# Optimization experiments

Hardware: AMD Instinct MI355X
Metric: run time of the kernel (lower is better)

## Reference

```python
import jax, jax.numpy as jnp
import numpy as np

PATCH_SIZE = 14.0
PIXEL_THRESHOLD = 5.0


def setup_inputs() -> dict:
    key = jax.random.key(0)
    k1, k2, k3, k4, k5 = jax.random.split(key, 5)
    B, N = 32, 1024
    src_pts = jax.random.uniform(k1, (B, N, 2), dtype=jnp.float32) * 32.0  # patch coords
    tar_pts = jax.random.uniform(k2, (B, N, 2), dtype=jnp.float32) * 32.0
    scores = jax.random.uniform(k3, (B, N), dtype=jnp.float32)
    relScale = 0.5 + jax.random.uniform(k4, (B, N), dtype=jnp.float32)  # positive scales
    theta = jax.random.uniform(k5, (B, N), dtype=jnp.float32) * 2.0 * np.pi
    relInplane = jnp.stack([jnp.cos(theta), jnp.sin(theta)], axis=-1)  # (B,N,2) cos,sin
    return {"src_pts": src_pts, "tar_pts": tar_pts, "scores": scores,
            "relScale": relScale, "relInplane": relInplane}


def _ransac_single(src, tar, score, scale, inplane):
    # src, tar: (N,2); score, scale: (N,); inplane: (N,2) = (cos, sin)
    N = src.shape[0]
    valid = src[:, 0] != -1.0  # (N,) sentinel mask from original forward
    s = src * PATCH_SIZE
    t = tar * PATCH_SIZE
    c, si = inplane[:, 0], inplane[:, 1]
    # R = [[c, -s], [s, c]] per candidate -> (N,2,2)
    R = jnp.stack([jnp.stack([c, -si], -1), jnp.stack([si, c], -1)], -2)
    A = scale[:, None, None] * R                          # (N,2,2) linear part
    trans = t - jnp.einsum('nij,nj->ni', A, s)            # (N,2) translation so A@s_n + t_n == t_n
    # candidate n applied to every point m (leave-one-out handled by masking diag)
    pred = jnp.einsum('nij,mj->nmi', A, s) + trans[:, None, :]   # (N,N,2)
    err = jnp.linalg.norm(pred - t[None, :, :], axis=-1)          # (N,N)
    not_self = ~jnp.eye(N, dtype=bool)
    inlier = (err <= PIXEL_THRESHOLD) & valid[None, :] & not_self  # (N,N)
    score_inl = jnp.sum(inlier * score[None, :], axis=1)           # (N,)
    score_inl = jnp.where(valid, score_inl, -1.0)
    best = jnp.argmax(score_inl)
    failed = score_inl[best] == 0.0
    M = (jnp.eye(3, dtype=src.dtype)
         .at[:2, :2].set(A[best])
         .at[:2, 2].set(trans[best]))
    # pack inliers of best candidate to the front (original index order preserved)
    inl = inlier[best]                                   # (N,) bool
    order = jnp.argsort(jnp.where(inl, 0, 1), stable=True)
    cnt = jnp.sum(inl)
    keep = jnp.arange(N) < cnt
    out_src = jnp.where(keep[:, None], src[order], -1.0)
    out_tar = jnp.where(keep[:, None], tar[order], -1.0)
    out_sc = jnp.where(keep, score[order], 0.0)
    return M, failed, out_src, out_tar, out_sc


def reference(src_pts, tar_pts, scores, relScale, relInplane):
    Ms, failed, inl_src, inl_tar, inl_sc = jax.vmap(_ransac_single)(
        src_pts, tar_pts, scores, relScale, relInplane)
    return Ms, failed, inl_src, inl_tar, inl_sc
```

## Files before the change

### kernel.cpp

```cpp
#include <hip/hip_runtime.h>

constexpr int BB = 32;
constexpr int NN = 1024;
constexpr int SPLIT = 16;
constexpr int HYP = 128;
#define PATCH 14.0f
#define THRSQ 25.0f

__global__ __launch_bounds__(1024) void ransac_score_kernel(
    const float* __restrict__ src, const float* __restrict__ tar,
    const float* __restrict__ scores, const float* __restrict__ relScale,
    const float* __restrict__ relInplane, float* __restrict__ score_inl)
{
#pragma clang fp contract(off)
    const int blocksPerBatch = NN / HYP;
    const int b   = blockIdx.x / blocksPerBatch;
    const int g   = blockIdx.x % blocksPerBatch;
    const int tid = threadIdx.x;
    const int wave = tid >> 6;
    const int lane = tid & 63;

    __shared__ float4 pts[NN];
    __shared__ float  sc[NN];
    __shared__ float  partial[SPLIT][HYP];

    const float* srcb = src + (size_t)b * NN * 2;
    const float* tarb = tar + (size_t)b * NN * 2;
    const float* scb  = scores + (size_t)b * NN;

    for (int i = tid; i < NN; i += 1024) {
        float2 s = ((const float2*)srcb)[i];
        float2 t = ((const float2*)tarb)[i];
        pts[i] = make_float4(s.x * PATCH, s.y * PATCH, t.x * PATCH, t.y * PATCH);
        sc[i]  = (s.x != -1.0f) ? scb[i] : 0.0f;
    }
    __syncthreads();

    const int n0l = lane, n1l = lane + 64;
    const size_t base = (size_t)b * NN + (size_t)g * HYP;

    const float sc0v = relScale[base + n0l];
    const float sc1v = relScale[base + n1l];
    const float2 ip0 = ((const float2*)relInplane)[base + n0l];
    const float2 ip1 = ((const float2*)relInplane)[base + n1l];

    const float a00_0 = sc0v * ip0.x, a01_0 = sc0v * (-ip0.y);
    const float a10_0 = sc0v * ip0.y, a11_0 = sc0v * ip0.x;
    const float a00_1 = sc1v * ip1.x, a01_1 = sc1v * (-ip1.y);
    const float a10_1 = sc1v * ip1.y, a11_1 = sc1v * ip1.x;

    const float4 P0 = pts[g * HYP + n0l];
    const float4 P1 = pts[g * HYP + n1l];
    const float trx0 = P0.z - (a00_0 * P0.x + a01_0 * P0.y);
    const float try0 = P0.w - (a10_0 * P0.x + a11_0 * P0.y);
    const float trx1 = P1.z - (a00_1 * P1.x + a01_1 * P1.y);
    const float try1 = P1.w - (a10_1 * P1.x + a11_1 * P1.y);

    float acc0 = 0.0f, acc1 = 0.0f;
    const int mBeg = wave * (NN / SPLIT);
#pragma unroll 4
    for (int mm = 0; mm < NN / SPLIT; ++mm) {
        const int m = mBeg + mm;
        const float4 q = pts[m];
        const float  w = sc[m];

        float px0 = a00_0 * q.x + a01_0 * q.y + trx0;
        float py0 = a10_0 * q.x + a11_0 * q.y + try0;
        float dx0 = px0 - q.z, dy0 = py0 - q.w;
        float e20 = dx0 * dx0 + dy0 * dy0;
        acc0 += (e20 <= THRSQ) ? w : 0.0f;

        float px1 = a00_1 * q.x + a01_1 * q.y + trx1;
        float py1 = a10_1 * q.x + a11_1 * q.y + try1;
        float dx1 = px1 - q.z, dy1 = py1 - q.w;
        float e21 = dx1 * dx1 + dy1 * dy1;
        acc1 += (e21 <= THRSQ) ? w : 0.0f;
    }
    partial[wave][n0l] = acc0;
    partial[wave][n1l] = acc1;
    __syncthreads();

    if (tid < HYP) {
        float p = 0.0f;
#pragma unroll
        for (int w = 0; w < SPLIT; ++w) p += partial[w][tid];
        p -= sc[g * HYP + tid];
        bool valid = (srcb[2 * (g * HYP + tid)] != -1.0f);
        score_inl[base + tid] = valid ? p : -1.0f;
    }
}

__global__ __launch_bounds__(1024) void ransac_select_kernel(
    const float* __restrict__ src, const float* __restrict__ tar,
    const float* __restrict__ scores, const float* __restrict__ relScale,
    const float* __restrict__ relInplane,
    const float* __restrict__ score_inl, float* __restrict__ out)
{
#pragma clang fp contract(off)
    const int b = blockIdx.x;
    const int tid = threadIdx.x;

    __shared__ float rval[NN];
    __shared__ int   ridx[NN];
    __shared__ float prm[6];
    __shared__ int   bestIdxSh;
    __shared__ int   wcnt[16], wbase[16];
    __shared__ float osx[NN], osy[NN], otx[NN], oty[NN], osc[NN];

    rval[tid] = score_inl[(size_t)b * NN + tid];
    ridx[tid] = tid;
    __syncthreads();
    for (int s = NN / 2; s > 0; s >>= 1) {
        if (tid < s) {
            float v1 = rval[tid],     v2 = rval[tid + s];
            int   i1 = ridx[tid],     i2 = ridx[tid + s];
            if (v2 > v1 || (v2 == v1 && i2 < i1)) { rval[tid] = v2; ridx[tid] = i2; }
        }
        __syncthreads();
    }

    if (tid == 0) {
        int best = ridx[0];
        bestIdxSh = best;
        size_t gi = (size_t)b * NN + best;
        float scale = relScale[gi];
        float c  = relInplane[gi * 2];
        float si = relInplane[gi * 2 + 1];
        float a00 = scale * c;
        float a01 = scale * (-si);
        float a10 = scale * si;
        float a11 = scale * c;
        float snx = src[gi * 2] * PATCH, sny = src[gi * 2 + 1] * PATCH;
        float tnx = tar[gi * 2] * PATCH, tny = tar[gi * 2 + 1] * PATCH;
        float trx = tnx - (a00 * snx + a01 * sny);
        float trY = tny - (a10 * snx + a11 * sny);
        prm[0] = a00; prm[1] = a01; prm[2] = a10; prm[3] = a11; prm[4] = trx; prm[5] = trY;

        float* M = out + (size_t)b * 9;
        M[0] = a00; M[1] = a01; M[2] = trx;
        M[3] = a10; M[4] = a11; M[5] = trY;
        M[6] = 0.0f; M[7] = 0.0f; M[8] = 1.0f;
        out[(size_t)BB * 9 + b] = (rval[0] == 0.0f) ? 1.0f : 0.0f;
    }
    __syncthreads();

    size_t gm = (size_t)b * NN + tid;
    float sxr = src[gm * 2], syr = src[gm * 2 + 1];
    float txr = tar[gm * 2], tyr = tar[gm * 2 + 1];
    float sx = sxr * PATCH, sy = syr * PATCH;
    float tx = txr * PATCH, ty = tyr * PATCH;
    float px = prm[0] * sx + prm[1] * sy + prm[4];
    float py = prm[2] * sx + prm[3] * sy + prm[5];
    float dx = px - tx, dy = py - ty;
    bool flag = (dx * dx + dy * dy <= THRSQ) && (sxr != -1.0f) && (tid != bestIdxSh);

    unsigned long long mask = __ballot(flag);
    int lane = tid & 63;
    int wave = tid >> 6;
    int posInWave = __popcll(mask & ((1ULL << lane) - 1ULL));
    if (lane == 0) wcnt[wave] = __popcll(mask);
    __syncthreads();
    if (tid < 16) {
        int s = 0;
        for (int i = 0; i < tid; ++i) s += wcnt[i];
        wbase[tid] = s;
    }
    __syncthreads();
    int pos = wbase[wave] + posInWave;

    osx[tid] = -1.0f; osy[tid] = -1.0f;
    otx[tid] = -1.0f; oty[tid] = -1.0f;
    osc[tid] = 0.0f;
    __syncthreads();
    if (flag) {
        osx[pos] = sxr; osy[pos] = syr;
        otx[pos] = txr; oty[pos] = tyr;
        osc[pos] = scores[gm];
    }
    __syncthreads();

    const size_t O_SRC = (size_t)BB * 9 + BB;
    const size_t O_TAR = O_SRC + (size_t)BB * NN * 2;
    const size_t O_SC  = O_TAR + (size_t)BB * NN * 2;
    out[O_SRC + gm * 2]     = osx[tid];
    out[O_SRC + gm * 2 + 1] = osy[tid];
    out[O_TAR + gm * 2]     = otx[tid];
    out[O_TAR + gm * 2 + 1] = oty[tid];
    out[O_SC  + gm]         = osc[tid];
}

extern "C" void kernel_launch(void* const* d_in, const int* in_sizes, int n_in,
                              void* d_out, int out_size, void* d_ws, size_t ws_size,
                              hipStream_t stream) {
    const float* src        = (const float*)d_in[0];
    const float* tar        = (const float*)d_in[1];
    const float* scores     = (const float*)d_in[2];
    const float* relScale   = (const float*)d_in[3];
    const float* relInplane = (const float*)d_in[4];
    float* out = (float*)d_out;
    float* score_inl = (float*)d_ws;

    ransac_score_kernel<<<BB * (NN / HYP), 1024, 0, stream>>>(
        src, tar, scores, relScale, relInplane, score_inl);
    ransac_select_kernel<<<BB, NN, 0, stream>>>(
        src, tar, scores, relScale, relInplane, score_inl, out);
}
```

Baseline: 21.54 us.

## Split scoring over point halves and use wave-shuffle argmax in select

The scoring kernel now splits the point set into two halves per hypothesis group, so the grid doubles to 512 blocks. Each block stages only half the points in shared memory, and the two partial score arrays are summed in the select kernel. Hypothesis parameters are loaded straight from global memory, overlapping with the shared-memory fill. The select kernel replaces its 10-step shared-memory tree reduction for argmax with wave shuffles and loads inputs once. The costs are a larger workspace and an extra partial-sum read.

```diff
diff --git a/kernel.cpp b/kernel.cpp
--- a/kernel.cpp
+++ b/kernel.cpp
@@ -2,67 +2,77 @@
 
 constexpr int BB = 32;
 constexpr int NN = 1024;
-constexpr int SPLIT = 16;
 constexpr int HYP = 128;
+constexpr int HALF = 512;
+constexpr int WAVES = 16;
+constexpr int ITERS = HALF / WAVES;
 #define PATCH 14.0f
 #define THRSQ 25.0f
 
-__global__ __launch_bounds__(1024) void ransac_score_kernel(
+__global__ __launch_bounds__(1024, 8) void ransac_score_kernel(
     const float* __restrict__ src, const float* __restrict__ tar,
     const float* __restrict__ scores, const float* __restrict__ relScale,
-    const float* __restrict__ relInplane, float* __restrict__ score_inl)
+    const float* __restrict__ relInplane, float* __restrict__ score_part)
 {
 #pragma clang fp contract(off)
-    const int blocksPerBatch = NN / HYP;
-    const int b   = blockIdx.x / blocksPerBatch;
-    const int g   = blockIdx.x % blocksPerBatch;
-    const int tid = threadIdx.x;
+    const int bid  = blockIdx.x;
+    const int half = bid & 1;
+    const int g    = (bid >> 1) & 7;
+    const int b    = bid >> 4;
+    const int tid  = threadIdx.x;
     const int wave = tid >> 6;
     const int lane = tid & 63;
 
-    __shared__ float4 pts[NN];
-    __shared__ float  sc[NN];
-    __shared__ float  partial[SPLIT][HYP];
-
-    const float* srcb = src + (size_t)b * NN * 2;
-    const float* tarb = tar + (size_t)b * NN * 2;
-    const float* scb  = scores + (size_t)b * NN;
-
-    for (int i = tid; i < NN; i += 1024) {
-        float2 s = ((const float2*)srcb)[i];
-        float2 t = ((const float2*)tarb)[i];
-        pts[i] = make_float4(s.x * PATCH, s.y * PATCH, t.x * PATCH, t.y * PATCH);
-        sc[i]  = (s.x != -1.0f) ? scb[i] : 0.0f;
-    }
-    __syncthreads();
-
-    const int n0l = lane, n1l = lane + 64;
-    const size_t base = (size_t)b * NN + (size_t)g * HYP;
-
-    const float sc0v = relScale[base + n0l];
-    const float sc1v = relScale[base + n1l];
-    const float2 ip0 = ((const float2*)relInplane)[base + n0l];
-    const float2 ip1 = ((const float2*)relInplane)[base + n1l];
-
-    const float a00_0 = sc0v * ip0.x, a01_0 = sc0v * (-ip0.y);
-    const float a10_0 = sc0v * ip0.y, a11_0 = sc0v * ip0.x;
-    const float a00_1 = sc1v * ip1.x, a01_1 = sc1v * (-ip1.y);
-    const float a10_1 = sc1v * ip1.y, a11_1 = sc1v * ip1.x;
-
-    const float4 P0 = pts[g * HYP + n0l];
-    const float4 P1 = pts[g * HYP + n1l];
-    const float trx0 = P0.z - (a00_0 * P0.x + a01_0 * P0.y);
-    const float try0 = P0.w - (a10_0 * P0.x + a11_0 * P0.y);
-    const float trx1 = P1.z - (a00_1 * P1.x + a01_1 * P1.y);
-    const float try1 = P1.w - (a10_1 * P1.x + a11_1 * P1.y);
+    __shared__ float4 pts[HALF];
+    __shared__ float  sc[HALF];
+    __shared__ float  partial[WAVES][HYP];
+
+    const float2* src2 = (const float2*)src + (size_t)b * NN;
+    const float2* tar2 = (const float2*)tar + (size_t)b * NN;
+    const float*  scb  = scores + (size_t)b * NN;
+    const int mOff = half * HALF;
+
+    if (tid < HALF) {
+        float2 s = src2[mOff + tid];
+        float2 t = tar2[mOff + tid];
+        pts[tid] = make_float4(s.x * PATCH, s.y * PATCH, t.x * PATCH, t.y * PATCH);
+        sc[tid]  = (s.x != -1.0f) ? scb[mOff + tid] : 0.0f;
+    }
+
+    const int n0 = g * HYP + lane;
+    const int n1 = n0 + 64;
+    const size_t nb = (size_t)b * NN;
+
+    const float sv0 = relScale[nb + n0];
+    const float sv1 = relScale[nb + n1];
+    const float2 ip0 = ((const float2*)relInplane)[nb + n0];
+    const float2 ip1 = ((const float2*)relInplane)[nb + n1];
+    float2 s0 = src2[n0], t0 = tar2[n0];
+    float2 s1 = src2[n1], t1 = tar2[n1];
+
+    const float a00_0 = sv0 * ip0.x, a01_0 = sv0 * (-ip0.y);
+    const float a10_0 = sv0 * ip0.y, a11_0 = sv0 * ip0.x;
+    const float a00_1 = sv1 * ip1.x, a01_1 = sv1 * (-ip1.y);
+    const float a10_1 = sv1 * ip1.y, a11_1 = sv1 * ip1.x;
+
+    const float P0x = s0.x * PATCH, P0y = s0.y * PATCH;
+    const float T0x = t0.x * PATCH, T0y = t0.y * PATCH;
+    const float P1x = s1.x * PATCH, P1y = s1.y * PATCH;
+    const float T1x = t1.x * PATCH, T1y = t1.y * PATCH;
+
+    const float trx0 = T0x - (a00_0 * P0x + a01_0 * P0y);
+    const float try0 = T0y - (a10_0 * P0x + a11_0 * P0y);
+    const float trx1 = T1x - (a00_1 * P1x + a01_1 * P1y);
+    const float try1 = T1y - (a10_1 * P1x + a11_1 * P1y);
+
+    __syncthreads();
 
     float acc0 = 0.0f, acc1 = 0.0f;
-    const int mBeg = wave * (NN / SPLIT);
-#pragma unroll 4
-    for (int mm = 0; mm < NN / SPLIT; ++mm) {
-        const int m = mBeg + mm;
-        const float4 q = pts[m];
-        const float  w = sc[m];
+    const int mBeg = wave * ITERS;
+#pragma unroll 8
+    for (int mm = 0; mm < ITERS; ++mm) {
+        const float4 q = pts[mBeg + mm];
+        const float  w = sc[mBeg + mm];
 
         float px0 = a00_0 * q.x + a01_0 * q.y + trx0;
         float py0 = a10_0 * q.x + a11_0 * q.y + try0;
@@ -76,17 +86,17 @@
         float e21 = dx1 * dx1 + dy1 * dy1;
         acc1 += (e21 <= THRSQ) ? w : 0.0f;
     }
-    partial[wave][n0l] = acc0;
-    partial[wave][n1l] = acc1;
+    partial[wave][lane]      = acc0;
+    partial[wave][lane + 64] = acc1;
     __syncthreads();
 
     if (tid < HYP) {
         float p = 0.0f;
 #pragma unroll
-        for (int w = 0; w < SPLIT; ++w) p += partial[w][tid];
-        p -= sc[g * HYP + tid];
-        bool valid = (srcb[2 * (g * HYP + tid)] != -1.0f);
-        score_inl[base + tid] = valid ? p : -1.0f;
+        for (int w = 0; w < WAVES; ++w) p += partial[w][tid];
+        const int n = g * HYP + tid;
+        if ((g >> 2) == half) p -= sc[n - mOff];
+        score_part[((size_t)half * BB + b) * NN + n] = p;
     }
 }
 
@@ -94,34 +104,56 @@
     const float* __restrict__ src, const float* __restrict__ tar,
     const float* __restrict__ scores, const float* __restrict__ relScale,
     const float* __restrict__ relInplane,
-    const float* __restrict__ score_inl, float* __restrict__ out)
+    const float* __restrict__ score_part, float* __restrict__ out)
 {
 #pragma clang fp contract(off)
     const int b = blockIdx.x;
     const int tid = threadIdx.x;
-
-    __shared__ float rval[NN];
-    __shared__ int   ridx[NN];
+    const int lane = tid & 63;
+    const int wave = tid >> 6;
+
+    __shared__ float wvalSh[16];
+    __shared__ int   widxSh[16];
     __shared__ float prm[6];
     __shared__ int   bestIdxSh;
+    __shared__ float bestValSh;
     __shared__ int   wcnt[16], wbase[16];
     __shared__ float osx[NN], osy[NN], otx[NN], oty[NN], osc[NN];
 
-    rval[tid] = score_inl[(size_t)b * NN + tid];
-    ridx[tid] = tid;
-    __syncthreads();
-    for (int s = NN / 2; s > 0; s >>= 1) {
-        if (tid < s) {
-            float v1 = rval[tid],     v2 = rval[tid + s];
-            int   i1 = ridx[tid],     i2 = ridx[tid + s];
-            if (v2 > v1 || (v2 == v1 && i2 < i1)) { rval[tid] = v2; ridx[tid] = i2; }
+    const size_t gm = (size_t)b * NN + tid;
+    const float2 s2 = ((const float2*)src)[gm];
+    const float2 t2 = ((const float2*)tar)[gm];
+    const float scin = scores[gm];
+
+    float val;
+    {
+        float p = score_part[(size_t)b * NN + tid]
+                + score_part[((size_t)BB + b) * NN + tid];
+        val = (s2.x != -1.0f) ? p : -1.0f;
+    }
+    int idx = tid;
+
+    for (int d = 1; d < 64; d <<= 1) {
+        float ov = __shfl_xor(val, d);
+        int   oi = __shfl_xor(idx, d);
+        if (ov > val || (ov == val && oi < idx)) { val = ov; idx = oi; }
+    }
+    if (lane == 0) { wvalSh[wave] = val; widxSh[wave] = idx; }
+    __syncthreads();
+    if (tid < 64) {
+        float v = (tid < 16) ? wvalSh[tid] : -1e30f;
+        int   i = (tid < 16) ? widxSh[tid] : 0x7fffffff;
+        for (int d = 1; d < 16; d <<= 1) {
+            float ov = __shfl_xor(v, d);
+            int   oi = __shfl_xor(i, d);
+            if (ov > v || (ov == v && oi < i)) { v = ov; i = oi; }
         }
-        __syncthreads();
-    }
+        if (tid == 0) { bestIdxSh = i; bestValSh = v; }
+    }
+    __syncthreads();
+    const int best = bestIdxSh;
 
     if (tid == 0) {
-        int best = ridx[0];
-        bestIdxSh = best;
         size_t gi = (size_t)b * NN + best;
         float scale = relScale[gi];
         float c  = relInplane[gi * 2];
@@ -140,23 +172,18 @@
         M[0] = a00; M[1] = a01; M[2] = trx;
         M[3] = a10; M[4] = a11; M[5] = trY;
         M[6] = 0.0f; M[7] = 0.0f; M[8] = 1.0f;
-        out[(size_t)BB * 9 + b] = (rval[0] == 0.0f) ? 1.0f : 0.0f;
-    }
-    __syncthreads();
-
-    size_t gm = (size_t)b * NN + tid;
-    float sxr = src[gm * 2], syr = src[gm * 2 + 1];
-    float txr = tar[gm * 2], tyr = tar[gm * 2 + 1];
-    float sx = sxr * PATCH, sy = syr * PATCH;
-    float tx = txr * PATCH, ty = tyr * PATCH;
+        out[(size_t)BB * 9 + b] = (bestValSh == 0.0f) ? 1.0f : 0.0f;
+    }
+    __syncthreads();
+
+    float sx = s2.x * PATCH, sy = s2.y * PATCH;
+    float tx = t2.x * PATCH, ty = t2.y * PATCH;
     float px = prm[0] * sx + prm[1] * sy + prm[4];
     float py = prm[2] * sx + prm[3] * sy + prm[5];
     float dx = px - tx, dy = py - ty;
-    bool flag = (dx * dx + dy * dy <= THRSQ) && (sxr != -1.0f) && (tid != bestIdxSh);
+    bool flag = (dx * dx + dy * dy <= THRSQ) && (s2.x != -1.0f) && (tid != best);
 
     unsigned long long mask = __ballot(flag);
-    int lane = tid & 63;
-    int wave = tid >> 6;
     int posInWave = __popcll(mask & ((1ULL << lane) - 1ULL));
     if (lane == 0) wcnt[wave] = __popcll(mask);
     __syncthreads();
@@ -173,9 +200,9 @@
     osc[tid] = 0.0f;
     __syncthreads();
     if (flag) {
-        osx[pos] = sxr; osy[pos] = syr;
-        otx[pos] = txr; oty[pos] = tyr;
-        osc[pos] = scores[gm];
+        osx[pos] = s2.x; osy[pos] = s2.y;
+        otx[pos] = t2.x; oty[pos] = t2.y;
+        osc[pos] = scin;
     }
     __syncthreads();
 
@@ -198,10 +225,10 @@
     const float* relScale   = (const float*)d_in[3];
     const float* relInplane = (const float*)d_in[4];
     float* out = (float*)d_out;
-    float* score_inl = (float*)d_ws;
-
-    ransac_score_kernel<<<BB * (NN / HYP), 1024, 0, stream>>>(
-        src, tar, scores, relScale, relInplane, score_inl);
+    float* score_part = (float*)d_ws;
+
+    ransac_score_kernel<<<BB * 8 * 2, 1024, 0, stream>>>(
+        src, tar, scores, relScale, relInplane, score_part);
     ransac_select_kernel<<<BB, NN, 0, stream>>>(
-        src, tar, scores, relScale, relInplane, score_inl, out);
+        src, tar, scores, relScale, relInplane, score_part, out);
 }
```

Measured after the change: 21.75 us. No clear change (+1.0%).
